# Performance work log

Measured on AMD Instinct MI355X. Metric: run time of the kernel, lower is better.

The kernel has to match this reference:

```python
import jax, jax.numpy as jnp
import numpy as np

B, A, G, D, H = 512, 32, 4, 1024, 16
DK = D // H            # 64
INNER = DK * H         # 1024 (== d_model since d_k defaulted)
P = A * G + 1          # 129 (with CLS token)


def _xavier(k, fout, fin):
    lim = np.sqrt(6.0 / (fin + fout)).astype(np.float32)
    return jax.random.uniform(k, (fout, fin), jnp.float32, -lim, lim)


def setup_inputs() -> dict:
    key = jax.random.key(0)
    ks = jax.random.split(key, 16)
    inp = {"x": jax.random.normal(ks[0], (B, P, D), jnp.float32)}
    names = ["q_ant", "k_ant", "v_ant", "q_freq", "k_freq", "v_freq"]
    for i, n in enumerate(names):
        inp["w_" + n] = _xavier(ks[1 + 2 * i], INNER, D if "ant" in n else INNER)
        inp["b_" + n] = jnp.zeros((INNER,), jnp.float32)
    inp["w_out"] = _xavier(ks[13], D, INNER)
    inp["b_out"] = jnp.zeros((D,), jnp.float32)
    return inp


def _sdpa(q, k, v):
    # q,k,v: [N, H, S, DK]
    scale = 1.0 / np.sqrt(DK).astype(np.float32)
    s = jnp.einsum('nhqd,nhkd->nhqk', q, k) * scale
    p = jax.nn.softmax(s, axis=-1)
    return jnp.einsum('nhqk,nhkd->nhqd', p, v)


def _heads(x, w, b, S):
    # x: [N, S, F] -> [N, H, S, DK]
    y = x @ w.T + b
    return y.reshape(-1, S, H, DK).transpose(0, 2, 1, 3)


def reference(x, w_q_ant, b_q_ant, w_k_ant, b_k_ant, w_v_ant, b_v_ant,
              w_q_freq, b_q_freq, w_k_freq, b_k_freq, w_v_freq, b_v_freq,
              w_out, b_out):
    Bv, Pv, Dv = x.shape
    cls_token = x[:, :1, :]                       # [B,1,D]
    grid = x[:, 1:, :].reshape(Bv, A, G, Dv)
    # ---- antenna-axis attention: batch over (B, freq_group) ----
    x_ant = grid.transpose(0, 2, 1, 3).reshape(Bv * G, A, Dv)
    q = _heads(x_ant, w_q_ant, b_q_ant, A)
    k = _heads(x_ant, w_k_ant, b_k_ant, A)
    v = _heads(x_ant, w_v_ant, b_v_ant, A)
    out_ant = _sdpa(q, k, v).transpose(0, 2, 1, 3).reshape(Bv * G, A, INNER)
    # ---- frequency-axis attention: batch over (B, antenna) ----
    x_freq = out_ant.reshape(Bv, G, A, INNER).transpose(0, 2, 1, 3).reshape(Bv * A, G, INNER)
    q = _heads(x_freq, w_q_freq, b_q_freq, G)
    k = _heads(x_freq, w_k_freq, b_k_freq, G)
    v = _heads(x_freq, w_v_freq, b_v_freq, G)
    out_freq = _sdpa(q, k, v).transpose(0, 2, 1, 3).reshape(Bv * A, G, INNER)
    # ---- output projection + CLS recombination (dropout=0 at eval) ----
    grid_flat = out_freq.reshape(Bv, A * G, INNER)
    grid_final = grid_flat @ w_out.T + b_out      # [B, A*G, D]
    grid_mean = grid_final.mean(axis=1, keepdims=True)
    cls_out = cls_token + grid_mean               # [B,1,D]
    grid_final = grid_final + cls_out
    return jnp.concatenate([cls_out, grid_final], axis=1)  # [B, P, D]
```

## Files before the change

### kernel.cpp

```cpp
#include <hip/hip_runtime.h>

typedef __attribute__((ext_vector_type(8))) short short8;
typedef __attribute__((ext_vector_type(4))) float f32x4;

#define DEV __device__ __forceinline__

DEV unsigned short f2bf(float f) {
  union { float f; unsigned u; } x; x.f = f;
  unsigned r = x.u + 0x7FFFu + ((x.u >> 16) & 1u);
  return (unsigned short)(r >> 16);
}
DEV float bf2f(short h) {
  union { unsigned u; float f; } x; x.u = ((unsigned)(unsigned short)h) << 16;
  return x.f;
}

DEV void gload16(const void* g, void* l) {
  __builtin_amdgcn_global_load_lds(
      (const __attribute__((address_space(1))) unsigned int*)g,
      (__attribute__((address_space(3))) unsigned int*)l, 16, 0, 0);
}

#define BARRIER() do { asm volatile("" ::: "memory"); \
  __builtin_amdgcn_s_barrier(); asm volatile("" ::: "memory"); } while (0)
#define WAIT_LGKM0() asm volatile("s_waitcnt lgkmcnt(0)" ::: "memory")
#define WAIT_VM8() asm volatile("s_waitcnt vmcnt(8)" ::: "memory")
#define WAIT_VM7() asm volatile("s_waitcnt vmcnt(7)" ::: "memory")
#define WAIT_VM0() asm volatile("s_waitcnt vmcnt(0)" ::: "memory")

struct CvtW { const float* s[7]; short* d[7]; };
__global__ __launch_bounds__(256) void cvt_weights(CvtW a) {
  int i = (blockIdx.x * 256 + threadIdx.x) * 8;
  int r = i >> 10, cix = i & 1023;
  int hh = r >> 6, dd = r & 63;
  #pragma unroll
  for (int m = 0; m < 7; ++m) {
    const float* s = a.s[m] + i;
    float4 v0 = *(const float4*)(s);
    float4 v1 = *(const float4*)(s + 4);
    short8 o;
    o[0] = (short)f2bf(v0.x); o[1] = (short)f2bf(v0.y);
    o[2] = (short)f2bf(v0.z); o[3] = (short)f2bf(v0.w);
    o[4] = (short)f2bf(v1.x); o[5] = (short)f2bf(v1.y);
    o[6] = (short)f2bf(v1.z); o[7] = (short)f2bf(v1.w);
    int dr = (m < 6) ? (hh * 192 + (m % 3) * 64 + dd) : r;
    *(short8*)(a.d[m] + (size_t)dr * 1024 + cix) = o;
  }
}

struct CvtB { const float* s[6]; float* d0; float* d1; };
__global__ __launch_bounds__(256) void cvt_bias(CvtB a) {
  int m = blockIdx.x;
  const float* s = a.s[m];
  float* dst = (m < 3) ? a.d0 : a.d1;
  int j = threadIdx.x * 4;
  int hh = j >> 6, dd = j & 63;
  float4 v = *(const float4*)(s + j);
  *(float4*)(dst + hh * 192 + (m % 3) * 64 + dd) = v;
}

__global__ __launch_bounds__(256) void permute_x(const float* __restrict__ x,
                                                 short* __restrict__ xa) {
  int m = blockIdx.x * 2 + (threadIdx.x >> 7);
  int a = m & 31, n = m >> 5;
  int g = n & 3, b = n >> 2;
  int c = (threadIdx.x & 127) * 8;
  size_t src = ((size_t)b * 129 + 1 + (size_t)a * 4 + g) * 1024 + c;
  float4 v0 = *(const float4*)(x + src);
  float4 v1 = *(const float4*)(x + src + 4);
  short8 o;
  o[0] = (short)f2bf(v0.x); o[1] = (short)f2bf(v0.y);
  o[2] = (short)f2bf(v0.z); o[3] = (short)f2bf(v0.w);
  o[4] = (short)f2bf(v1.x); o[5] = (short)f2bf(v1.y);
  o[6] = (short)f2bf(v1.z); o[7] = (short)f2bf(v1.w);
  *(short8*)(xa + (size_t)m * 1024 + c) = o;
}

#define PH_MFMA3(q) do { \
  __builtin_amdgcn_s_setprio(1); \
  _Pragma("unroll") for (int kk = 0; kk < 2; ++kk) \
    _Pragma("unroll") for (int m = 0; m < 2; ++m) \
      _Pragma("unroll") for (int nf = 0; nf < 3; ++nf) \
        acc[(q)*2+m][nf] = __builtin_amdgcn_mfma_f32_16x16x32_bf16( \
            af[m][kk], bf3[nf][kk], acc[(q)*2+m][nf], 0, 0, 0); \
  __builtin_amdgcn_s_setprio(0); } while (0)

#define LOAD_A(q) do { \
  const char* pa = base + aRdBase + ((q)*32 + l15) * 128; \
  af[0][0] = *(const short8*)(pa + swz0); \
  af[0][1] = *(const short8*)(pa + swz1); \
  af[1][0] = *(const short8*)(pa + 2048 + swz0); \
  af[1][1] = *(const short8*)(pa + 2048 + swz1); \
} while (0)

template <int STAGE>
__global__ __launch_bounds__(512, 2)
void gemm_attn(const short* __restrict__ A, const short* __restrict__ Bm,
               const float* __restrict__ bias, short* __restrict__ Outp, int K) {
  extern __shared__ char ls[];
  int nwg = gridDim.x;
  int bid = blockIdx.x;
  bid = (bid & 7) * (nwg >> 3) + (bid >> 3);
  int tm = (bid >> 4) << 8;
  int hh = bid & 15;
  int t = threadIdx.x;
  int lane = t & 63, w = t >> 6;
  int wm = w >> 2, wn = w & 3;
  int l15 = lane & 15, l4 = lane >> 4;
  int cg = (lane & 7) ^ ((lane >> 3) & 7);

  const short* aS[2][2];
  #pragma unroll
  for (int h = 0; h < 2; ++h)
    #pragma unroll
    for (int i = 0; i < 2; ++i) {
      int r = h * 128 + (w * 2 + i) * 8 + (lane >> 3);
      aS[h][i] = A + (size_t)(tm + r) * K + cg * 8;
    }
  const short* bS[3];
  #pragma unroll
  for (int j = 0; j < 3; ++j) {
    int r = j * 64 + w * 8 + (lane >> 3);
    bS[j] = Bm + (size_t)(hh * 192 + r) * K + cg * 8;
  }
  int dstOff = (w * 2) * 1024;
  auto stageA = [&](int c, int kt) {
    #pragma unroll
    for (int h = 0; h < 2; ++h)
      #pragma unroll
      for (int i = 0; i < 2; ++i)
        gload16(aS[h][i] + kt * 64, ls + c * 65536 + h * 16384 + dstOff + i * 1024);
  };
  auto stageB = [&](int c, int kt, int j) {
    gload16(bS[j] + kt * 64, ls + c * 65536 + 32768 + j * 8192 + w * 1024);
  };
  int aRdBase = wm * 16384;
  int swz0 = ((l4 ^ (l15 & 7)) << 4);
  int swz1 = swz0 ^ 64;

  f32x4 acc[8][3];
  #pragma unroll
  for (int m = 0; m < 8; ++m)
    #pragma unroll
    for (int n = 0; n < 3; ++n) acc[m][n] = (f32x4){0.f, 0.f, 0.f, 0.f};

  int NT = K >> 6;
  stageB(0, 0, 0); stageB(0, 0, 1); stageB(0, 0, 2); stageA(0, 0);
  stageB(1, 1, 0); stageB(1, 1, 1); stageB(1, 1, 2); stageA(1, 1);
  WAIT_VM7();
  BARRIER();

  for (int kt = 0; kt < NT; ++kt) {
    int c = kt & 1;
    const char* base = ls + c * 65536;
    bool stg = (kt + 2) < NT;
    short8 bf3[3][2], af[2][2];
    #pragma unroll
    for (int nf = 0; nf < 3; ++nf) {
      const char* p = base + 32768 + (wn * 48 + nf * 16 + l15) * 128;
      bf3[nf][0] = *(const short8*)(p + swz0);
      bf3[nf][1] = *(const short8*)(p + swz1);
    }
    LOAD_A(0);
    BARRIER();
    PH_MFMA3(0);
    BARRIER();
    if (stg) { stageB(c, kt + 2, 0); stageB(c, kt + 2, 1); }
    LOAD_A(1);
    BARRIER();
    PH_MFMA3(1);
    BARRIER();
    if (stg) stageB(c, kt + 2, 2);
    LOAD_A(2);
    BARRIER();
    PH_MFMA3(2);
    BARRIER();
    LOAD_A(3);
    WAIT_LGKM0();
    BARRIER();
    if (stg) stageA(c, kt + 2);
    PH_MFMA3(3);
    if (stg) { WAIT_VM7(); } else { WAIT_VM0(); }
    BARRIER();
  }

  const float* bb = bias + hh * 192;
  #pragma unroll
  for (int nf = 0; nf < 3; ++nf) {
    int col = wn * 48 + nf * 16 + l15;
    float bv = bb[col];
    #pragma unroll
    for (int mf = 0; mf < 8; ++mf)
      #pragma unroll
      for (int j = 0; j < 4; ++j) {
        int row = wm * 128 + mf * 16 + l4 * 4 + j;
        *(short*)(ls + row * 400 + col * 2) = (short)f2bf(acc[mf][nf][j] + bv);
      }
  }
  WAIT_LGKM0();
  BARRIER();

  if constexpr (STAGE == 1) {
    const char* qk = ls + (size_t)(w * 32) * 400;
    short8 qf[2][2], kf[2][2];
    #pragma unroll
    for (int mt = 0; mt < 2; ++mt)
      #pragma unroll
      for (int kk = 0; kk < 2; ++kk) {
        int row = mt * 16 + l15;
        qf[mt][kk] = *(const short8*)(qk + row * 400 + (kk * 32 + l4 * 8) * 2);
        kf[mt][kk] = *(const short8*)(qk + row * 400 + 128 + (kk * 32 + l4 * 8) * 2);
      }
    f32x4 sf[2][2];
    #pragma unroll
    for (int mt = 0; mt < 2; ++mt)
      #pragma unroll
      for (int nt = 0; nt < 2; ++nt) sf[mt][nt] = (f32x4){0.f, 0.f, 0.f, 0.f};
    #pragma unroll
    for (int kk = 0; kk < 2; ++kk)
      #pragma unroll
      for (int mt = 0; mt < 2; ++mt)
        #pragma unroll
        for (int nt = 0; nt < 2; ++nt)
          sf[mt][nt] = __builtin_amdgcn_mfma_f32_16x16x32_bf16(qf[mt][kk], kf[nt][kk], sf[mt][nt], 0, 0, 0);

    short* Pw = (short*)(ls + 102400 + w * 2560);
    #pragma unroll
    for (int mt = 0; mt < 2; ++mt)
      #pragma unroll
      for (int j = 0; j < 4; ++j) {
        float a0 = sf[mt][0][j] * 0.125f;
        float a1 = sf[mt][1][j] * 0.125f;
        float mx = fmaxf(a0, a1);
        mx = fmaxf(mx, __shfl_xor(mx, 1));
        mx = fmaxf(mx, __shfl_xor(mx, 2));
        mx = fmaxf(mx, __shfl_xor(mx, 4));
        mx = fmaxf(mx, __shfl_xor(mx, 8));
        float e0 = __expf(a0 - mx), e1 = __expf(a1 - mx);
        float sm = e0 + e1;
        sm += __shfl_xor(sm, 1);
        sm += __shfl_xor(sm, 2);
        sm += __shfl_xor(sm, 4);
        sm += __shfl_xor(sm, 8);
        float inv = 1.0f / sm;
        int row = mt * 16 + l4 * 4 + j;
        Pw[row * 40 + l15]      = (short)f2bf(e0 * inv);
        Pw[row * 40 + 16 + l15] = (short)f2bf(e1 * inv);
      }
    WAIT_LGKM0();

    short8 pa[2], vb[4];
    pa[0] = *(const short8*)(Pw + l15 * 40 + l4 * 8);
    pa[1] = *(const short8*)(Pw + (16 + l15) * 40 + l4 * 8);
    #pragma unroll
    for (int nt = 0; nt < 4; ++nt) {
      short8 v;
      #pragma unroll
      for (int j = 0; j < 8; ++j)
        v[j] = *(const short*)(qk + (l4 * 8 + j) * 400 + 256 + (nt * 16 + l15) * 2);
      vb[nt] = v;
    }
    f32x4 of[2][4];
    #pragma unroll
    for (int mt = 0; mt < 2; ++mt)
      #pragma unroll
      for (int nt = 0; nt < 4; ++nt) of[mt][nt] = (f32x4){0.f, 0.f, 0.f, 0.f};
    #pragma unroll
    for (int mt = 0; mt < 2; ++mt)
      #pragma unroll
      for (int nt = 0; nt < 4; ++nt)
        of[mt][nt] = __builtin_amdgcn_mfma_f32_16x16x32_bf16(pa[mt], vb[nt], of[mt][nt], 0, 0, 0);

    int nn = (tm >> 5) + w;
    int b = nn >> 2, g = nn & 3;
    #pragma unroll
    for (int mt = 0; mt < 2; ++mt)
      #pragma unroll
      for (int j = 0; j < 4; ++j) {
        int q = mt * 16 + l4 * 4 + j;
        size_t orow = (((size_t)b * 32 + q) * 4 + g) * 1024 + hh * 64;
        #pragma unroll
        for (int nt = 0; nt < 4; ++nt)
          Outp[orow + nt * 16 + l15] = (short)f2bf(of[mt][nt][j]);
      }
  } else {
    int gi = t >> 3, s = t & 7, gq = s >> 1, dh = s & 1;
    const char* grp = ls + (size_t)(gi * 4) * 400;
    short8 q8[4];
    #pragma unroll
    for (int c = 0; c < 4; ++c)
      q8[c] = *(const short8*)(grp + gq * 400 + dh * 64 + c * 16);
    float dot[4];
    #pragma unroll
    for (int k = 0; k < 4; ++k) {
      float p = 0.f;
      #pragma unroll
      for (int c = 0; c < 4; ++c) {
        short8 k8 = *(const short8*)(grp + k * 400 + 128 + dh * 64 + c * 16);
        #pragma unroll
        for (int j = 0; j < 8; ++j) p += bf2f(q8[c][j]) * bf2f(k8[j]);
      }
      p += __shfl_xor(p, 1);
      dot[k] = p * 0.125f;
    }
    float mx = fmaxf(fmaxf(dot[0], dot[1]), fmaxf(dot[2], dot[3]));
    float e[4], sm = 0.f;
    #pragma unroll
    for (int k = 0; k < 4; ++k) { e[k] = __expf(dot[k] - mx); sm += e[k]; }
    float inv = 1.0f / sm;
    float o[32];
    #pragma unroll
    for (int j = 0; j < 32; ++j) o[j] = 0.f;
    #pragma unroll
    for (int k = 0; k < 4; ++k) {
      float pk = e[k] * inv;
      #pragma unroll
      for (int c = 0; c < 4; ++c) {
        short8 v8 = *(const short8*)(grp + k * 400 + 256 + dh * 64 + c * 16);
        #pragma unroll
        for (int j = 0; j < 8; ++j) o[c * 8 + j] += pk * bf2f(v8[j]);
      }
    }
    int n4 = ((tm >> 2) + gi) * 4 + gq;
    short* orow = Outp + (size_t)n4 * 1024 + hh * 64 + dh * 32;
    #pragma unroll
    for (int c = 0; c < 4; ++c) {
      short8 a8;
      #pragma unroll
      for (int j = 0; j < 8; ++j) a8[j] = (short)f2bf(o[c * 8 + j]);
      *(short8*)(orow + c * 8) = a8;
    }
  }
}

#define PH_MFMA(q) do { \
  __builtin_amdgcn_s_setprio(1); \
  _Pragma("unroll") for (int kk = 0; kk < 2; ++kk) \
    _Pragma("unroll") for (int m = 0; m < 2; ++m) \
      _Pragma("unroll") for (int nf = 0; nf < 4; ++nf) \
        acc[(q)*2+m][nf] = __builtin_amdgcn_mfma_f32_16x16x32_bf16( \
            af[m][kk], bf[nf][kk], acc[(q)*2+m][nf], 0, 0, 0); \
  __builtin_amdgcn_s_setprio(0); } while (0)

__global__ __launch_bounds__(512, 2)
void gemm_out(const short* __restrict__ A, const short* __restrict__ Bm,
              const float* __restrict__ bias, const float* __restrict__ x,
              float* __restrict__ Out, int M, int N, int K) {
  extern __shared__ char ls[];
  int nbn = N >> 8;
  int nwg = gridDim.x;
  int bid = blockIdx.x;
  bid = (bid & 7) * (nwg >> 3) + (bid >> 3);
  int tm = (bid / nbn) << 8;
  int tn = (bid % nbn) << 8;
  int t = threadIdx.x;
  int lane = t & 63, w = t >> 6;
  int wm = w >> 2, wn = w & 3;
  int l15 = lane & 15, l4 = lane >> 4;
  int cg = (lane & 7) ^ ((lane >> 3) & 7);
  const short* aS[2][2];
  const short* bS[2][2];
  #pragma unroll
  for (int h = 0; h < 2; ++h)
    #pragma unroll
    for (int i = 0; i < 2; ++i) {
      int r = h * 128 + (w * 2 + i) * 8 + (lane >> 3);
      aS[h][i] = A + (size_t)(tm + r) * K + cg * 8;
      bS[h][i] = Bm + (size_t)(tn + r) * K + cg * 8;
    }
  int dstOff = (w * 2) * 1024;
  auto stageA = [&](int c, int kt) {
    #pragma unroll
    for (int h = 0; h < 2; ++h)
      #pragma unroll
      for (int i = 0; i < 2; ++i)
        gload16(aS[h][i] + kt * 64, ls + c * 65536 + h * 16384 + dstOff + i * 1024);
  };
  auto stageB = [&](int c, int kt, int h) {
    #pragma unroll
    for (int i = 0; i < 2; ++i)
      gload16(bS[h][i] + kt * 64, ls + c * 65536 + 32768 + h * 16384 + dstOff + i * 1024);
  };
  int aRdBase = wm * 16384;
  int bRdBase = 32768 + (wn >> 1) * 16384;
  int bRow0 = (wn & 1) * 64;
  int swz0 = ((l4 ^ (l15 & 7)) << 4);
  int swz1 = swz0 ^ 64;
  f32x4 acc[8][4];
  #pragma unroll
  for (int m = 0; m < 8; ++m)
    #pragma unroll
    for (int n = 0; n < 4; ++n) acc[m][n] = (f32x4){0.f, 0.f, 0.f, 0.f};
  int NT = K >> 6;
  stageB(0, 0, 0); stageB(0, 0, 1); stageA(0, 0);
  stageB(1, 1, 0); stageB(1, 1, 1); stageA(1, 1);
  WAIT_VM8();
  BARRIER();
  for (int kt = 0; kt < NT; ++kt) {
    int c = kt & 1;
    const char* base = ls + c * 65536;
    bool stg = (kt + 2) < NT;
    short8 bf[4][2], af[2][2];
    #pragma unroll
    for (int nf = 0; nf < 4; ++nf) {
      const char* p = base + bRdBase + (bRow0 + nf * 16 + l15) * 128;
      bf[nf][0] = *(const short8*)(p + swz0);
      bf[nf][1] = *(const short8*)(p + swz1);
    }
    LOAD_A(0);
    BARRIER();
    PH_MFMA(0);
    BARRIER();
    if (stg) stageB(c, kt + 2, 0);
    LOAD_A(1);
    BARRIER();
    PH_MFMA(1);
    BARRIER();
    if (stg) stageB(c, kt + 2, 1);
    LOAD_A(2);
    BARRIER();
    PH_MFMA(2);
    BARRIER();
    LOAD_A(3);
    WAIT_LGKM0();
    BARRIER();
    if (stg) stageA(c, kt + 2);
    PH_MFMA(3);
    if (stg) { WAIT_VM8(); } else { WAIT_VM0(); }
    BARRIER();
  }
  int b = (tm >> 7) + wm;
  #pragma unroll
  for (int nf = 0; nf < 4; ++nf) {
    int colg = tn + wn * 64 + nf * 16 + l15;
    float bv = bias[colg];
    float s = 0.f;
    #pragma unroll
    for (int mf = 0; mf < 8; ++mf)
      #pragma unroll
      for (int j = 0; j < 4; ++j) s += acc[mf][nf][j];
    s += 32.0f * bv;
    s += __shfl_xor(s, 16);
    s += __shfl_xor(s, 32);
    float cls = x[(size_t)b * 129 * 1024 + colg] + s * (1.0f / 128.0f);
    if (l4 == 0)
      Out[((size_t)b * 129) * 1024 + colg] = cls;
    #pragma unroll
    for (int mf = 0; mf < 8; ++mf) {
      #pragma unroll
      for (int j = 0; j < 4; ++j) {
        int tok = mf * 16 + l4 * 4 + j;
        Out[((size_t)b * 129 + 1 + tok) * 1024 + colg] = acc[mf][nf][j] + bv + cls;
      }
    }
  }
}

extern "C" void kernel_launch(void* const* d_in, const int* in_sizes, int n_in,
                              void* d_out, int out_size, void* d_ws, size_t ws_size,
                              hipStream_t stream) {
  const float* x        = (const float*)d_in[0];
  const float* w_q_ant  = (const float*)d_in[1];
  const float* b_q_ant  = (const float*)d_in[2];
  const float* w_k_ant  = (const float*)d_in[3];
  const float* b_k_ant  = (const float*)d_in[4];
  const float* w_v_ant  = (const float*)d_in[5];
  const float* b_v_ant  = (const float*)d_in[6];
  const float* w_q_freq = (const float*)d_in[7];
  const float* b_q_freq = (const float*)d_in[8];
  const float* w_k_freq = (const float*)d_in[9];
  const float* b_k_freq = (const float*)d_in[10];
  const float* w_v_freq = (const float*)d_in[11];
  const float* b_v_freq = (const float*)d_in[12];
  const float* w_out    = (const float*)d_in[13];
  const float* b_out    = (const float*)d_in[14];

  char* ws = (char*)d_ws;
  size_t off = 0;
  auto carve = [&](size_t bytes) {
    char* p = ws + off;
    off += (bytes + 255) & ~(size_t)255;
    return p;
  };
  short* wcat_ant  = (short*)carve((size_t)3072 * 1024 * 2);
  short* wcat_freq = (short*)carve((size_t)3072 * 1024 * 2);
  short* wout_bf   = (short*)carve((size_t)1024 * 1024 * 2);
  float* bcat_ant  = (float*)carve(3072 * 4);
  float* bcat_freq = (float*)carve(3072 * 4);
  short* bufA = (short*)carve((size_t)65536 * 1024 * 2);
  short* bufF = (short*)carve((size_t)65536 * 1024 * 2);
  short* bufG = (short*)carve((size_t)65536 * 1024 * 2);
  (void)ws_size; (void)in_sizes; (void)n_in; (void)out_size;

  hipFuncSetAttribute((const void*)gemm_attn<1>,
                      hipFuncAttributeMaxDynamicSharedMemorySize, 131072);
  hipFuncSetAttribute((const void*)gemm_attn<2>,
                      hipFuncAttributeMaxDynamicSharedMemorySize, 131072);
  hipFuncSetAttribute((const void*)gemm_out,
                      hipFuncAttributeMaxDynamicSharedMemorySize, 131072);

  CvtW cw;
  cw.s[0] = w_q_ant;  cw.s[1] = w_k_ant;  cw.s[2] = w_v_ant;
  cw.s[3] = w_q_freq; cw.s[4] = w_k_freq; cw.s[5] = w_v_freq;
  cw.s[6] = w_out;
  cw.d[0] = wcat_ant;  cw.d[1] = wcat_ant;  cw.d[2] = wcat_ant;
  cw.d[3] = wcat_freq; cw.d[4] = wcat_freq; cw.d[5] = wcat_freq;
  cw.d[6] = wout_bf;
  cvt_weights<<<512, 256, 0, stream>>>(cw);

  CvtB cb;
  cb.s[0] = b_q_ant;  cb.s[1] = b_k_ant;  cb.s[2] = b_v_ant;
  cb.s[3] = b_q_freq; cb.s[4] = b_k_freq; cb.s[5] = b_v_freq;
  cb.d0 = bcat_ant; cb.d1 = bcat_freq;
  cvt_bias<<<6, 256, 0, stream>>>(cb);

  permute_x<<<32768, 256, 0, stream>>>(x, bufA);

  gemm_attn<1><<<4096, 512, 131072, stream>>>(bufA, wcat_ant, bcat_ant, bufF, 1024);
  gemm_attn<2><<<4096, 512, 131072, stream>>>(bufF, wcat_freq, bcat_freq, bufG, 1024);
  gemm_out<<<1024, 512, 131072, stream>>>(bufG, wout_bf, b_out, x, (float*)d_out,
                                          65536, 1024, 1024);
}
```

Baseline: 1.206 ms.

## Fuse x permute and bf16 conversion into first GEMM, restructure prefetch pipeline

Removes the separate permute_x kernel and its 128MB bf16 intermediate by having stage-1 GEMM load fp32 x directly via registers, convert to bf16 and write to LDS. The multi-stage prefetch (two tiles ahead with partial vmcnt waits) is replaced by a one-tile-ahead double buffer with full vmcnt(0) waits in all GEMMs. This saves a full pass over x, but stage 1 now reads fp32 (twice the bytes, through VGPRs rather than direct-to-LDS loads), and the shallower pipeline may expose more load latency.

```diff
diff --git a/kernel.cpp b/kernel.cpp
--- a/kernel.cpp
+++ b/kernel.cpp
@@ -24,8 +24,6 @@
 #define BARRIER() do { asm volatile("" ::: "memory"); \
   __builtin_amdgcn_s_barrier(); asm volatile("" ::: "memory"); } while (0)
 #define WAIT_LGKM0() asm volatile("s_waitcnt lgkmcnt(0)" ::: "memory")
-#define WAIT_VM8() asm volatile("s_waitcnt vmcnt(8)" ::: "memory")
-#define WAIT_VM7() asm volatile("s_waitcnt vmcnt(7)" ::: "memory")
 #define WAIT_VM0() asm volatile("s_waitcnt vmcnt(0)" ::: "memory")
 
 struct CvtW { const float* s[7]; short* d[7]; };
@@ -59,23 +57,6 @@
   *(float4*)(dst + hh * 192 + (m % 3) * 64 + dd) = v;
 }
 
-__global__ __launch_bounds__(256) void permute_x(const float* __restrict__ x,
-                                                 short* __restrict__ xa) {
-  int m = blockIdx.x * 2 + (threadIdx.x >> 7);
-  int a = m & 31, n = m >> 5;
-  int g = n & 3, b = n >> 2;
-  int c = (threadIdx.x & 127) * 8;
-  size_t src = ((size_t)b * 129 + 1 + (size_t)a * 4 + g) * 1024 + c;
-  float4 v0 = *(const float4*)(x + src);
-  float4 v1 = *(const float4*)(x + src + 4);
-  short8 o;
-  o[0] = (short)f2bf(v0.x); o[1] = (short)f2bf(v0.y);
-  o[2] = (short)f2bf(v0.z); o[3] = (short)f2bf(v0.w);
-  o[4] = (short)f2bf(v1.x); o[5] = (short)f2bf(v1.y);
-  o[6] = (short)f2bf(v1.z); o[7] = (short)f2bf(v1.w);
-  *(short8*)(xa + (size_t)m * 1024 + c) = o;
-}
-
 #define PH_MFMA3(q) do { \
   __builtin_amdgcn_s_setprio(1); \
   _Pragma("unroll") for (int kk = 0; kk < 2; ++kk) \
@@ -95,7 +76,7 @@
 
 template <int STAGE>
 __global__ __launch_bounds__(512, 2)
-void gemm_attn(const short* __restrict__ A, const short* __restrict__ Bm,
+void gemm_attn(const void* __restrict__ Asrc, const short* __restrict__ Bm,
                const float* __restrict__ bias, short* __restrict__ Outp, int K) {
   extern __shared__ char ls[];
   int nwg = gridDim.x;
@@ -110,12 +91,19 @@
   int cg = (lane & 7) ^ ((lane >> 3) & 7);
 
   const short* aS[2][2];
+  const float* aX[2][2];
   #pragma unroll
   for (int h = 0; h < 2; ++h)
     #pragma unroll
     for (int i = 0; i < 2; ++i) {
       int r = h * 128 + (w * 2 + i) * 8 + (lane >> 3);
-      aS[h][i] = A + (size_t)(tm + r) * K + cg * 8;
+      int m = tm + r;
+      if constexpr (STAGE == 1) {
+        int a = m & 31, n = m >> 5, g = n & 3, b = n >> 2;
+        aX[h][i] = (const float*)Asrc + (size_t)(b * 129 + 1 + a * 4 + g) * 1024 + cg * 8;
+      } else {
+        aS[h][i] = (const short*)Asrc + (size_t)m * K + cg * 8;
+      }
     }
   const short* bS[3];
   #pragma unroll
@@ -123,17 +111,46 @@
     int r = j * 64 + w * 8 + (lane >> 3);
     bS[j] = Bm + (size_t)(hh * 192 + r) * K + cg * 8;
   }
-  int dstOff = (w * 2) * 1024;
-  auto stageA = [&](int c, int kt) {
+
+  auto stageB3 = [&](int cbuf, int kt) {
+    #pragma unroll
+    for (int j = 0; j < 3; ++j)
+      gload16(bS[j] + kt * 64, ls + cbuf * 65536 + 32768 + j * 8192 + w * 1024);
+  };
+  auto stageA2 = [&](int cbuf, int kt) {
     #pragma unroll
     for (int h = 0; h < 2; ++h)
       #pragma unroll
       for (int i = 0; i < 2; ++i)
-        gload16(aS[h][i] + kt * 64, ls + c * 65536 + h * 16384 + dstOff + i * 1024);
-  };
-  auto stageB = [&](int c, int kt, int j) {
-    gload16(bS[j] + kt * 64, ls + c * 65536 + 32768 + j * 8192 + w * 1024);
-  };
+        gload16(aS[h][i] + kt * 64,
+                ls + cbuf * 65536 + h * 16384 + (w * 2 + i) * 1024 + lane * 16);
+  };
+  float4 fv[4][2];
+  auto loadA1 = [&](int kt) {
+    #pragma unroll
+    for (int h = 0; h < 2; ++h)
+      #pragma unroll
+      for (int i = 0; i < 2; ++i) {
+        const float* p = aX[h][i] + kt * 64;
+        fv[h * 2 + i][0] = *(const float4*)p;
+        fv[h * 2 + i][1] = *(const float4*)(p + 4);
+      }
+  };
+  auto writeA1 = [&](int cbuf) {
+    #pragma unroll
+    for (int h = 0; h < 2; ++h)
+      #pragma unroll
+      for (int i = 0; i < 2; ++i) {
+        float4 v0 = fv[h * 2 + i][0], v1 = fv[h * 2 + i][1];
+        short8 o;
+        o[0] = (short)f2bf(v0.x); o[1] = (short)f2bf(v0.y);
+        o[2] = (short)f2bf(v0.z); o[3] = (short)f2bf(v0.w);
+        o[4] = (short)f2bf(v1.x); o[5] = (short)f2bf(v1.y);
+        o[6] = (short)f2bf(v1.z); o[7] = (short)f2bf(v1.w);
+        *(short8*)(ls + cbuf * 65536 + h * 16384 + (w * 2 + i) * 1024 + lane * 16) = o;
+      }
+  };
+
   int aRdBase = wm * 16384;
   int swz0 = ((l4 ^ (l15 & 7)) << 4);
   int swz1 = swz0 ^ 64;
@@ -145,15 +162,20 @@
     for (int n = 0; n < 3; ++n) acc[m][n] = (f32x4){0.f, 0.f, 0.f, 0.f};
 
   int NT = K >> 6;
-  stageB(0, 0, 0); stageB(0, 0, 1); stageB(0, 0, 2); stageA(0, 0);
-  stageB(1, 1, 0); stageB(1, 1, 1); stageB(1, 1, 2); stageA(1, 1);
-  WAIT_VM7();
+  stageB3(0, 0);
+  if constexpr (STAGE == 1) {
+    loadA1(0); writeA1(0);
+    WAIT_VM0(); WAIT_LGKM0();
+  } else {
+    stageA2(0, 0);
+    WAIT_VM0();
+  }
   BARRIER();
 
   for (int kt = 0; kt < NT; ++kt) {
     int c = kt & 1;
     const char* base = ls + c * 65536;
-    bool stg = (kt + 2) < NT;
+    bool stg = (kt + 1) < NT;
     short8 bf3[3][2], af[2][2];
     #pragma unroll
     for (int nf = 0; nf < 3; ++nf) {
@@ -162,25 +184,30 @@
       bf3[nf][1] = *(const short8*)(p + swz1);
     }
     LOAD_A(0);
+    if (stg) {
+      stageB3(c ^ 1, kt + 1);
+      if constexpr (STAGE == 1) loadA1(kt + 1);
+    }
     BARRIER();
     PH_MFMA3(0);
     BARRIER();
-    if (stg) { stageB(c, kt + 2, 0); stageB(c, kt + 2, 1); }
     LOAD_A(1);
+    if constexpr (STAGE == 2) { if (stg) stageA2(c ^ 1, kt + 1); }
     BARRIER();
     PH_MFMA3(1);
     BARRIER();
-    if (stg) stageB(c, kt + 2, 2);
     LOAD_A(2);
+    if constexpr (STAGE == 1) { if (stg) writeA1(c ^ 1); }
     BARRIER();
     PH_MFMA3(2);
     BARRIER();
     LOAD_A(3);
-    WAIT_LGKM0();
-    BARRIER();
-    if (stg) stageA(c, kt + 2);
+    BARRIER();
     PH_MFMA3(3);
-    if (stg) { WAIT_VM7(); } else { WAIT_VM0(); }
+    if (stg) {
+      WAIT_VM0();
+      if constexpr (STAGE == 1) WAIT_LGKM0();
+    }
     BARRIER();
   }
 
@@ -369,17 +396,19 @@
       bS[h][i] = Bm + (size_t)(tn + r) * K + cg * 8;
     }
   int dstOff = (w * 2) * 1024;
-  auto stageA = [&](int c, int kt) {
+  auto stageA = [&](int cbuf, int kt) {
     #pragma unroll
     for (int h = 0; h < 2; ++h)
       #pragma unroll
       for (int i = 0; i < 2; ++i)
-        gload16(aS[h][i] + kt * 64, ls + c * 65536 + h * 16384 + dstOff + i * 1024);
-  };
-  auto stageB = [&](int c, int kt, int h) {
-    #pragma unroll
-    for (int i = 0; i < 2; ++i)
-      gload16(bS[h][i] + kt * 64, ls + c * 65536 + 32768 + h * 16384 + dstOff + i * 1024);
+        gload16(aS[h][i] + kt * 64, ls + cbuf * 65536 + h * 16384 + dstOff + i * 1024);
+  };
+  auto stageB = [&](int cbuf, int kt) {
+    #pragma unroll
+    for (int h = 0; h < 2; ++h)
+      #pragma unroll
+      for (int i = 0; i < 2; ++i)
+        gload16(bS[h][i] + kt * 64, ls + cbuf * 65536 + 32768 + h * 16384 + dstOff + i * 1024);
   };
   int aRdBase = wm * 16384;
   int bRdBase = 32768 + (wn >> 1) * 16384;
@@ -392,14 +421,13 @@
     #pragma unroll
     for (int n = 0; n < 4; ++n) acc[m][n] = (f32x4){0.f, 0.f, 0.f, 0.f};
   int NT = K >> 6;
-  stageB(0, 0, 0); stageB(0, 0, 1); stageA(0, 0);
-  stageB(1, 1, 0); stageB(1, 1, 1); stageA(1, 1);
-  WAIT_VM8();
+  stageB(0, 0); stageA(0, 0);
+  WAIT_VM0();
   BARRIER();
   for (int kt = 0; kt < NT; ++kt) {
     int c = kt & 1;
     const char* base = ls + c * 65536;
-    bool stg = (kt + 2) < NT;
+    bool stg = (kt + 1) < NT;
     short8 bf[4][2], af[2][2];
     #pragma unroll
     for (int nf = 0; nf < 4; ++nf) {
@@ -408,25 +436,23 @@
       bf[nf][1] = *(const short8*)(p + swz1);
     }
     LOAD_A(0);
+    if (stg) stageB(c ^ 1, kt + 1);
     BARRIER();
     PH_MFMA(0);
     BARRIER();
-    if (stg) stageB(c, kt + 2, 0);
     LOAD_A(1);
+    if (stg) stageA(c ^ 1, kt + 1);
     BARRIER();
     PH_MFMA(1);
     BARRIER();
-    if (stg) stageB(c, kt + 2, 1);
     LOAD_A(2);
     BARRIER();
     PH_MFMA(2);
     BARRIER();
     LOAD_A(3);
-    WAIT_LGKM0();
-    BARRIER();
-    if (stg) stageA(c, kt + 2);
+    BARRIER();
     PH_MFMA(3);
-    if (stg) { WAIT_VM8(); } else { WAIT_VM0(); }
+    if (stg) WAIT_VM0();
     BARRIER();
   }
   int b = (tm >> 7) + wm;
@@ -487,7 +513,6 @@
   short* wout_bf   = (short*)carve((size_t)1024 * 1024 * 2);
   float* bcat_ant  = (float*)carve(3072 * 4);
   float* bcat_freq = (float*)carve(3072 * 4);
-  short* bufA = (short*)carve((size_t)65536 * 1024 * 2);
   short* bufF = (short*)carve((size_t)65536 * 1024 * 2);
   short* bufG = (short*)carve((size_t)65536 * 1024 * 2);
   (void)ws_size; (void)in_sizes; (void)n_in; (void)out_size;
@@ -514,9 +539,7 @@
   cb.d0 = bcat_ant; cb.d1 = bcat_freq;
   cvt_bias<<<6, 256, 0, stream>>>(cb);
 
-  permute_x<<<32768, 256, 0, stream>>>(x, bufA);
-
-  gemm_attn<1><<<4096, 512, 131072, stream>>>(bufA, wcat_ant, bcat_ant, bufF, 1024);
+  gemm_attn<1><<<4096, 512, 131072, stream>>>(x, wcat_ant, bcat_ant, bufF, 1024);
   gemm_attn<2><<<4096, 512, 131072, stream>>>(bufF, wcat_freq, bcat_freq, bufG, 1024);
   gemm_out<<<1024, 512, 131072, stream>>>(bufG, wout_bf, b_out, x, (float*)d_out,
                                           65536, 1024, 1024);
```

Result: slower. 1.445 ms (+19.8%).

## Run QKV-attention GEMM with 1024 threads per block, halving per-wave M tile

Applied to the files above, without the earlier changes.

The fused QKV-projection/attention kernel now launches 1024 threads (16 waves) per block instead of 512 with two blocks per CU. Each wave computes a 64x48 slice instead of 128x48, so there are half as many accumulator registers per wave, and the global-to-LDS staging work is redistributed across 16 waves. The attention epilogue still uses only the first 8 waves or 512 threads, leaving half the block idle there. Since LDS use per block is unchanged at 128KB, the intent appears to be the same wave count per CU with fewer registers per wave and one larger block, traded against barriers that must now synchronise 16 waves.

```diff
diff --git a/kernel.cpp b/kernel.cpp
--- a/kernel.cpp
+++ b/kernel.cpp
@@ -25,7 +25,7 @@
   __builtin_amdgcn_s_barrier(); asm volatile("" ::: "memory"); } while (0)
 #define WAIT_LGKM0() asm volatile("s_waitcnt lgkmcnt(0)" ::: "memory")
 #define WAIT_VM8() asm volatile("s_waitcnt vmcnt(8)" ::: "memory")
-#define WAIT_VM7() asm volatile("s_waitcnt vmcnt(7)" ::: "memory")
+#define WAIT_VM3() asm volatile("s_waitcnt vmcnt(3)" ::: "memory")
 #define WAIT_VM0() asm volatile("s_waitcnt vmcnt(0)" ::: "memory")
 
 struct CvtW { const float* s[7]; short* d[7]; };
@@ -79,22 +79,19 @@
 #define PH_MFMA3(q) do { \
   __builtin_amdgcn_s_setprio(1); \
   _Pragma("unroll") for (int kk = 0; kk < 2; ++kk) \
-    _Pragma("unroll") for (int m = 0; m < 2; ++m) \
-      _Pragma("unroll") for (int nf = 0; nf < 3; ++nf) \
-        acc[(q)*2+m][nf] = __builtin_amdgcn_mfma_f32_16x16x32_bf16( \
-            af[m][kk], bf3[nf][kk], acc[(q)*2+m][nf], 0, 0, 0); \
+    _Pragma("unroll") for (int nf = 0; nf < 3; ++nf) \
+      acc[q][nf] = __builtin_amdgcn_mfma_f32_16x16x32_bf16( \
+          af[kk], bf3[nf][kk], acc[q][nf], 0, 0, 0); \
   __builtin_amdgcn_s_setprio(0); } while (0)
 
-#define LOAD_A(q) do { \
-  const char* pa = base + aRdBase + ((q)*32 + l15) * 128; \
-  af[0][0] = *(const short8*)(pa + swz0); \
-  af[0][1] = *(const short8*)(pa + swz1); \
-  af[1][0] = *(const short8*)(pa + 2048 + swz0); \
-  af[1][1] = *(const short8*)(pa + 2048 + swz1); \
+#define LOAD_A16(q) do { \
+  const char* pa = base + wm * 8192 + ((q)*16 + l15) * 128; \
+  af[0] = *(const short8*)(pa + swz0); \
+  af[1] = *(const short8*)(pa + swz1); \
 } while (0)
 
 template <int STAGE>
-__global__ __launch_bounds__(512, 2)
+__global__ __launch_bounds__(1024)
 void gemm_attn(const short* __restrict__ A, const short* __restrict__ Bm,
                const float* __restrict__ bias, short* __restrict__ Outp, int K) {
   extern __shared__ char ls[];
@@ -109,78 +106,68 @@
   int l15 = lane & 15, l4 = lane >> 4;
   int cg = (lane & 7) ^ ((lane >> 3) & 7);
 
-  const short* aS[2][2];
-  #pragma unroll
-  for (int h = 0; h < 2; ++h)
-    #pragma unroll
-    for (int i = 0; i < 2; ++i) {
-      int r = h * 128 + (w * 2 + i) * 8 + (lane >> 3);
-      aS[h][i] = A + (size_t)(tm + r) * K + cg * 8;
-    }
-  const short* bS[3];
-  #pragma unroll
-  for (int j = 0; j < 3; ++j) {
-    int r = j * 64 + w * 8 + (lane >> 3);
-    bS[j] = Bm + (size_t)(hh * 192 + r) * K + cg * 8;
-  }
-  int dstOff = (w * 2) * 1024;
+  const short* aS[2];
+  #pragma unroll
+  for (int s = 0; s < 2; ++s) {
+    int r = (w + s * 16) * 8 + (lane >> 3);
+    aS[s] = A + (size_t)(tm + r) * K + cg * 8;
+  }
+  const short* bS0 = Bm + (size_t)(hh * 192 + w * 8 + (lane >> 3)) * K + cg * 8;
+  const short* bS1 = Bm + (size_t)(hh * 192 + ((w & 7) + 16) * 8 + (lane >> 3)) * K + cg * 8;
+
   auto stageA = [&](int c, int kt) {
-    #pragma unroll
-    for (int h = 0; h < 2; ++h)
-      #pragma unroll
-      for (int i = 0; i < 2; ++i)
-        gload16(aS[h][i] + kt * 64, ls + c * 65536 + h * 16384 + dstOff + i * 1024);
+    gload16(aS[0] + kt * 64, ls + c * 65536 + w * 1024);
+    gload16(aS[1] + kt * 64, ls + c * 65536 + (w + 16) * 1024);
   };
-  auto stageB = [&](int c, int kt, int j) {
-    gload16(bS[j] + kt * 64, ls + c * 65536 + 32768 + j * 8192 + w * 1024);
+  auto stageB = [&](int c, int kt) {
+    gload16(bS0 + kt * 64, ls + c * 65536 + 32768 + w * 1024);
+    if (w < 8) gload16(bS1 + kt * 64, ls + c * 65536 + 32768 + (16 + w) * 1024);
   };
-  int aRdBase = wm * 16384;
   int swz0 = ((l4 ^ (l15 & 7)) << 4);
   int swz1 = swz0 ^ 64;
 
-  f32x4 acc[8][3];
-  #pragma unroll
-  for (int m = 0; m < 8; ++m)
+  f32x4 acc[4][3];
+  #pragma unroll
+  for (int m = 0; m < 4; ++m)
     #pragma unroll
     for (int n = 0; n < 3; ++n) acc[m][n] = (f32x4){0.f, 0.f, 0.f, 0.f};
 
   int NT = K >> 6;
-  stageB(0, 0, 0); stageB(0, 0, 1); stageB(0, 0, 2); stageA(0, 0);
-  stageB(1, 1, 0); stageB(1, 1, 1); stageB(1, 1, 2); stageA(1, 1);
-  WAIT_VM7();
+  stageB(0, 0); stageA(0, 0);
+  stageB(1, 1); stageA(1, 1);
+  WAIT_VM3();
   BARRIER();
 
   for (int kt = 0; kt < NT; ++kt) {
     int c = kt & 1;
     const char* base = ls + c * 65536;
     bool stg = (kt + 2) < NT;
-    short8 bf3[3][2], af[2][2];
+    short8 bf3[3][2], af[2];
     #pragma unroll
     for (int nf = 0; nf < 3; ++nf) {
       const char* p = base + 32768 + (wn * 48 + nf * 16 + l15) * 128;
       bf3[nf][0] = *(const short8*)(p + swz0);
       bf3[nf][1] = *(const short8*)(p + swz1);
     }
-    LOAD_A(0);
+    LOAD_A16(0);
     BARRIER();
     PH_MFMA3(0);
     BARRIER();
-    if (stg) { stageB(c, kt + 2, 0); stageB(c, kt + 2, 1); }
-    LOAD_A(1);
+    if (stg) stageB(c, kt + 2);
+    LOAD_A16(1);
     BARRIER();
     PH_MFMA3(1);
     BARRIER();
-    if (stg) stageB(c, kt + 2, 2);
-    LOAD_A(2);
+    LOAD_A16(2);
     BARRIER();
     PH_MFMA3(2);
     BARRIER();
-    LOAD_A(3);
+    LOAD_A16(3);
     WAIT_LGKM0();
     BARRIER();
     if (stg) stageA(c, kt + 2);
     PH_MFMA3(3);
-    if (stg) { WAIT_VM7(); } else { WAIT_VM0(); }
+    if (stg) { WAIT_VM3(); } else { WAIT_VM0(); }
     BARRIER();
   }
 
@@ -190,10 +177,10 @@
     int col = wn * 48 + nf * 16 + l15;
     float bv = bb[col];
     #pragma unroll
-    for (int mf = 0; mf < 8; ++mf)
+    for (int mf = 0; mf < 4; ++mf)
       #pragma unroll
       for (int j = 0; j < 4; ++j) {
-        int row = wm * 128 + mf * 16 + l4 * 4 + j;
+        int row = wm * 64 + mf * 16 + l4 * 4 + j;
         *(short*)(ls + row * 400 + col * 2) = (short)f2bf(acc[mf][nf][j] + bv);
       }
   }
@@ -201,134 +188,138 @@
   BARRIER();
 
   if constexpr (STAGE == 1) {
-    const char* qk = ls + (size_t)(w * 32) * 400;
-    short8 qf[2][2], kf[2][2];
-    #pragma unroll
-    for (int mt = 0; mt < 2; ++mt)
-      #pragma unroll
-      for (int kk = 0; kk < 2; ++kk) {
-        int row = mt * 16 + l15;
-        qf[mt][kk] = *(const short8*)(qk + row * 400 + (kk * 32 + l4 * 8) * 2);
-        kf[mt][kk] = *(const short8*)(qk + row * 400 + 128 + (kk * 32 + l4 * 8) * 2);
+    if (w < 8) {
+      const char* qk = ls + (size_t)(w * 32) * 400;
+      short8 qf[2][2], kf[2][2];
+      #pragma unroll
+      for (int mt = 0; mt < 2; ++mt)
+        #pragma unroll
+        for (int kk = 0; kk < 2; ++kk) {
+          int row = mt * 16 + l15;
+          qf[mt][kk] = *(const short8*)(qk + row * 400 + (kk * 32 + l4 * 8) * 2);
+          kf[mt][kk] = *(const short8*)(qk + row * 400 + 128 + (kk * 32 + l4 * 8) * 2);
+        }
+      f32x4 sf[2][2];
+      #pragma unroll
+      for (int mt = 0; mt < 2; ++mt)
+        #pragma unroll
+        for (int nt = 0; nt < 2; ++nt) sf[mt][nt] = (f32x4){0.f, 0.f, 0.f, 0.f};
+      #pragma unroll
+      for (int kk = 0; kk < 2; ++kk)
+        #pragma unroll
+        for (int mt = 0; mt < 2; ++mt)
+          #pragma unroll
+          for (int nt = 0; nt < 2; ++nt)
+            sf[mt][nt] = __builtin_amdgcn_mfma_f32_16x16x32_bf16(qf[mt][kk], kf[nt][kk], sf[mt][nt], 0, 0, 0);
+
+      short* Pw = (short*)(ls + 102400 + w * 2560);
+      #pragma unroll
+      for (int mt = 0; mt < 2; ++mt)
+        #pragma unroll
+        for (int j = 0; j < 4; ++j) {
+          float a0 = sf[mt][0][j] * 0.125f;
+          float a1 = sf[mt][1][j] * 0.125f;
+          float mx = fmaxf(a0, a1);
+          mx = fmaxf(mx, __shfl_xor(mx, 1));
+          mx = fmaxf(mx, __shfl_xor(mx, 2));
+          mx = fmaxf(mx, __shfl_xor(mx, 4));
+          mx = fmaxf(mx, __shfl_xor(mx, 8));
+          float e0 = __expf(a0 - mx), e1 = __expf(a1 - mx);
+          float sm = e0 + e1;
+          sm += __shfl_xor(sm, 1);
+          sm += __shfl_xor(sm, 2);
+          sm += __shfl_xor(sm, 4);
+          sm += __shfl_xor(sm, 8);
+          float inv = 1.0f / sm;
+          int row = mt * 16 + l4 * 4 + j;
+          Pw[row * 40 + l15]      = (short)f2bf(e0 * inv);
+          Pw[row * 40 + 16 + l15] = (short)f2bf(e1 * inv);
+        }
+      WAIT_LGKM0();
+
+      short8 pa[2], vb[4];
+      pa[0] = *(const short8*)(Pw + l15 * 40 + l4 * 8);
+      pa[1] = *(const short8*)(Pw + (16 + l15) * 40 + l4 * 8);
+      #pragma unroll
+      for (int nt = 0; nt < 4; ++nt) {
+        short8 v;
+        #pragma unroll
+        for (int j = 0; j < 8; ++j)
+          v[j] = *(const short*)(qk + (l4 * 8 + j) * 400 + 256 + (nt * 16 + l15) * 2);
+        vb[nt] = v;
       }
-    f32x4 sf[2][2];
-    #pragma unroll
-    for (int mt = 0; mt < 2; ++mt)
-      #pragma unroll
-      for (int nt = 0; nt < 2; ++nt) sf[mt][nt] = (f32x4){0.f, 0.f, 0.f, 0.f};
-    #pragma unroll
-    for (int kk = 0; kk < 2; ++kk)
+      f32x4 of[2][4];
       #pragma unroll
       for (int mt = 0; mt < 2; ++mt)
         #pragma unroll
-        for (int nt = 0; nt < 2; ++nt)
-          sf[mt][nt] = __builtin_amdgcn_mfma_f32_16x16x32_bf16(qf[mt][kk], kf[nt][kk], sf[mt][nt], 0, 0, 0);
-
-    short* Pw = (short*)(ls + 102400 + w * 2560);
-    #pragma unroll
-    for (int mt = 0; mt < 2; ++mt)
-      #pragma unroll
-      for (int j = 0; j < 4; ++j) {
-        float a0 = sf[mt][0][j] * 0.125f;
-        float a1 = sf[mt][1][j] * 0.125f;
-        float mx = fmaxf(a0, a1);
-        mx = fmaxf(mx, __shfl_xor(mx, 1));
-        mx = fmaxf(mx, __shfl_xor(mx, 2));
-        mx = fmaxf(mx, __shfl_xor(mx, 4));
-        mx = fmaxf(mx, __shfl_xor(mx, 8));
-        float e0 = __expf(a0 - mx), e1 = __expf(a1 - mx);
-        float sm = e0 + e1;
-        sm += __shfl_xor(sm, 1);
-        sm += __shfl_xor(sm, 2);
-        sm += __shfl_xor(sm, 4);
-        sm += __shfl_xor(sm, 8);
-        float inv = 1.0f / sm;
-        int row = mt * 16 + l4 * 4 + j;
-        Pw[row * 40 + l15]      = (short)f2bf(e0 * inv);
-        Pw[row * 40 + 16 + l15] = (short)f2bf(e1 * inv);
+        for (int nt = 0; nt < 4; ++nt) of[mt][nt] = (f32x4){0.f, 0.f, 0.f, 0.f};
+      #pragma unroll
+      for (int mt = 0; mt < 2; ++mt)
+        #pragma unroll
+        for (int nt = 0; nt < 4; ++nt)
+          of[mt][nt] = __builtin_amdgcn_mfma_f32_16x16x32_bf16(pa[mt], vb[nt], of[mt][nt], 0, 0, 0);
+
+      int nn = (tm >> 5) + w;
+      int b = nn >> 2, g = nn & 3;
+      #pragma unroll
+      for (int mt = 0; mt < 2; ++mt)
+        #pragma unroll
+        for (int j = 0; j < 4; ++j) {
+          int q = mt * 16 + l4 * 4 + j;
+          size_t orow = (((size_t)b * 32 + q) * 4 + g) * 1024 + hh * 64;
+          #pragma unroll
+          for (int nt = 0; nt < 4; ++nt)
+            Outp[orow + nt * 16 + l15] = (short)f2bf(of[mt][nt][j]);
+        }
+    }
+  } else {
+    if (t < 512) {
+      int gi = t >> 3, s = t & 7, gq = s >> 1, dh = s & 1;
+      const char* grp = ls + (size_t)(gi * 4) * 400;
+      short8 q8[4];
+      #pragma unroll
+      for (int c = 0; c < 4; ++c)
+        q8[c] = *(const short8*)(grp + gq * 400 + dh * 64 + c * 16);
+      float dot[4];
+      #pragma unroll
+      for (int k = 0; k < 4; ++k) {
+        float p = 0.f;
+        #pragma unroll
+        for (int c = 0; c < 4; ++c) {
+          short8 k8 = *(const short8*)(grp + k * 400 + 128 + dh * 64 + c * 16);
+          #pragma unroll
+          for (int j = 0; j < 8; ++j) p += bf2f(q8[c][j]) * bf2f(k8[j]);
+        }
+        p += __shfl_xor(p, 1);
+        dot[k] = p * 0.125f;
       }
-    WAIT_LGKM0();
-
-    short8 pa[2], vb[4];
-    pa[0] = *(const short8*)(Pw + l15 * 40 + l4 * 8);
-    pa[1] = *(const short8*)(Pw + (16 + l15) * 40 + l4 * 8);
-    #pragma unroll
-    for (int nt = 0; nt < 4; ++nt) {
-      short8 v;
-      #pragma unroll
-      for (int j = 0; j < 8; ++j)
-        v[j] = *(const short*)(qk + (l4 * 8 + j) * 400 + 256 + (nt * 16 + l15) * 2);
-      vb[nt] = v;
-    }
-    f32x4 of[2][4];
-    #pragma unroll
-    for (int mt = 0; mt < 2; ++mt)
-      #pragma unroll
-      for (int nt = 0; nt < 4; ++nt) of[mt][nt] = (f32x4){0.f, 0.f, 0.f, 0.f};
-    #pragma unroll
-    for (int mt = 0; mt < 2; ++mt)
-      #pragma unroll
-      for (int nt = 0; nt < 4; ++nt)
-        of[mt][nt] = __builtin_amdgcn_mfma_f32_16x16x32_bf16(pa[mt], vb[nt], of[mt][nt], 0, 0, 0);
-
-    int nn = (tm >> 5) + w;
-    int b = nn >> 2, g = nn & 3;
-    #pragma unroll
-    for (int mt = 0; mt < 2; ++mt)
-      #pragma unroll
-      for (int j = 0; j < 4; ++j) {
-        int q = mt * 16 + l4 * 4 + j;
-        size_t orow = (((size_t)b * 32 + q) * 4 + g) * 1024 + hh * 64;
-        #pragma unroll
-        for (int nt = 0; nt < 4; ++nt)
-          Outp[orow + nt * 16 + l15] = (short)f2bf(of[mt][nt][j]);
+      float mx = fmaxf(fmaxf(dot[0], dot[1]), fmaxf(dot[2], dot[3]));
+      float e[4], sm = 0.f;
+      #pragma unroll
+      for (int k = 0; k < 4; ++k) { e[k] = __expf(dot[k] - mx); sm += e[k]; }
+      float inv = 1.0f / sm;
+      float o[32];
+      #pragma unroll
+      for (int j = 0; j < 32; ++j) o[j] = 0.f;
+      #pragma unroll
+      for (int k = 0; k < 4; ++k) {
+        float pk = e[k] * inv;
+        #pragma unroll
+        for (int c = 0; c < 4; ++c) {
+          short8 v8 = *(const short8*)(grp + k * 400 + 256 + dh * 64 + c * 16);
+          #pragma unroll
+          for (int j = 0; j < 8; ++j) o[c * 8 + j] += pk * bf2f(v8[j]);
+        }
       }
-  } else {
-    int gi = t >> 3, s = t & 7, gq = s >> 1, dh = s & 1;
-    const char* grp = ls + (size_t)(gi * 4) * 400;
-    short8 q8[4];
-    #pragma unroll
-    for (int c = 0; c < 4; ++c)
-      q8[c] = *(const short8*)(grp + gq * 400 + dh * 64 + c * 16);
-    float dot[4];
-    #pragma unroll
-    for (int k = 0; k < 4; ++k) {
-      float p = 0.f;
+      int n4 = ((tm >> 2) + gi) * 4 + gq;
+      short* orow = Outp + (size_t)n4 * 1024 + hh * 64 + dh * 32;
       #pragma unroll
       for (int c = 0; c < 4; ++c) {
-        short8 k8 = *(const short8*)(grp + k * 400 + 128 + dh * 64 + c * 16);
-        #pragma unroll
-        for (int j = 0; j < 8; ++j) p += bf2f(q8[c][j]) * bf2f(k8[j]);
+        short8 a8;
+        #pragma unroll
+        for (int j = 0; j < 8; ++j) a8[j] = (short)f2bf(o[c * 8 + j]);
+        *(short8*)(orow + c * 8) = a8;
       }
-      p += __shfl_xor(p, 1);
-      dot[k] = p * 0.125f;
-    }
-    float mx = fmaxf(fmaxf(dot[0], dot[1]), fmaxf(dot[2], dot[3]));
-    float e[4], sm = 0.f;
-    #pragma unroll
-    for (int k = 0; k < 4; ++k) { e[k] = __expf(dot[k] - mx); sm += e[k]; }
-    float inv = 1.0f / sm;
-    float o[32];
-    #pragma unroll
-    for (int j = 0; j < 32; ++j) o[j] = 0.f;
-    #pragma unroll
-    for (int k = 0; k < 4; ++k) {
-      float pk = e[k] * inv;
-      #pragma unroll
-      for (int c = 0; c < 4; ++c) {
-        short8 v8 = *(const short8*)(grp + k * 400 + 256 + dh * 64 + c * 16);
-        #pragma unroll
-        for (int j = 0; j < 8; ++j) o[c * 8 + j] += pk * bf2f(v8[j]);
-      }
-    }
-    int n4 = ((tm >> 2) + gi) * 4 + gq;
-    short* orow = Outp + (size_t)n4 * 1024 + hh * 64 + dh * 32;
-    #pragma unroll
-    for (int c = 0; c < 4; ++c) {
-      short8 a8;
-      #pragma unroll
-      for (int j = 0; j < 8; ++j) a8[j] = (short)f2bf(o[c * 8 + j]);
-      *(short8*)(orow + c * 8) = a8;
     }
   }
 }
@@ -341,6 +332,14 @@
         acc[(q)*2+m][nf] = __builtin_amdgcn_mfma_f32_16x16x32_bf16( \
             af[m][kk], bf[nf][kk], acc[(q)*2+m][nf], 0, 0, 0); \
   __builtin_amdgcn_s_setprio(0); } while (0)
+
+#define LOAD_A(q) do { \
+  const char* pa = base + aRdBase + ((q)*32 + l15) * 128; \
+  af[0][0] = *(const short8*)(pa + swz0); \
+  af[0][1] = *(const short8*)(pa + swz1); \
+  af[1][0] = *(const short8*)(pa + 2048 + swz0); \
+  af[1][1] = *(const short8*)(pa + 2048 + swz1); \
+} while (0)
 
 __global__ __launch_bounds__(512, 2)
 void gemm_out(const short* __restrict__ A, const short* __restrict__ Bm,
@@ -516,8 +515,8 @@
 
   permute_x<<<32768, 256, 0, stream>>>(x, bufA);
 
-  gemm_attn<1><<<4096, 512, 131072, stream>>>(bufA, wcat_ant, bcat_ant, bufF, 1024);
-  gemm_attn<2><<<4096, 512, 131072, stream>>>(bufF, wcat_freq, bcat_freq, bufG, 1024);
+  gemm_attn<1><<<4096, 1024, 131072, stream>>>(bufA, wcat_ant, bcat_ant, bufF, 1024);
+  gemm_attn<2><<<4096, 1024, 131072, stream>>>(bufF, wcat_freq, bcat_freq, bufG, 1024);
   gemm_out<<<1024, 512, 131072, stream>>>(bufG, wout_bf, b_out, x, (float*)d_out,
                                           65536, 1024, 1024);
 }
```

After: 1.220 ms. Within noise of the previous version (+1.2%).
